# Kernel optimization log

Hardware: AMD Instinct MI355X
Metric: run time of the kernel (lower is better)

Reference implementation:

```python
import jax, jax.numpy as jnp
import numpy as np

MIN_STD = 0.1

def _lin(x, W, b):
    return x @ W.T + b


def setup_inputs() -> dict:
    B, T, H, L, E, A = 256, 128, 2048, 256, 1024, 32
    key = jax.random.key(0)
    ks = jax.random.split(key, 40)
    def w(i, shape, s=0.02):
        return (jax.random.normal(ks[i], shape, jnp.float32) * s)
    z = lambda n: jnp.zeros((n,), jnp.float32)
    return {
        "prev_stochastic_state": w(0, (B, L), 1.0),
        "prev_hidden": w(1, (B, H), 1.0),
        "encoded_obs": w(2, (B, T, E), 1.0),
        "actions": w(3, (B, T, A), 1.0),
        "noise_prior": w(4, (B, T, L), 1.0),
        "noise_post": w(5, (B, T, L), 1.0),
        # fc_embed_state_action
        "W_embed": w(6, (H, L + A)), "b_embed": z(H),
        # GRUCell (torch layout: 3H rows = [r; z; n])
        "W_ih": w(7, (3 * H, H)), "b_ih": z(3 * H),
        "W_hh": w(8, (3 * H, H)), "b_hh": z(3 * H),
        # prior MLP (200-dim) + heads
        "Wp1": w(9, (200, H)), "bp1": z(200),
        "Wp2": w(10, (200, 200)), "bp2": z(200),
        "Wpm": w(11, (L, 200)), "bpm": z(L),
        "Wps": w(12, (L, 200)), "bps": z(L),
        # posterior MLP (200-dim) + heads
        "Wq1": w(13, (200, H + E)), "bq1": z(200),
        "Wq2": w(14, (200, 200)), "bq2": z(200),
        "Wqm": w(15, (L, 200)), "bqm": z(L),
        "Wqs": w(16, (L, 200)), "bqs": z(L),
        # reward head
        "Wr1": w(17, (200, L + H)), "br1": z(200),
        "Wr2": w(18, (200, 200)), "br2": z(200),
        "Wr3": w(19, (1, 200)), "br3": z(1),
    }


def reference(prev_stochastic_state, prev_hidden, encoded_obs, actions,
              noise_prior, noise_post,
              W_embed, b_embed, W_ih, b_ih, W_hh, b_hh,
              Wp1, bp1, Wp2, bp2, Wpm, bpm, Wps, bps,
              Wq1, bq1, Wq2, bq2, Wqm, bqm, Wqs, bqs,
              Wr1, br1, Wr2, br2, Wr3, br3):
    def gru(x, h):
        gi = x @ W_ih.T + b_ih          # [B, 3H]
        gh = h @ W_hh.T + b_hh
        i_r, i_z, i_n = jnp.split(gi, 3, axis=-1)
        h_r, h_z, h_n = jnp.split(gh, 3, axis=-1)
        r = jax.nn.sigmoid(i_r + h_r)
        z = jax.nn.sigmoid(i_z + h_z)
        n = jnp.tanh(i_n + r * h_n)
        return (1.0 - z) * n + z * h

    def step(carry, xs):
        post, h = carry
        enc_t, act_t, np_t, nq_t = xs
        emb = jax.nn.relu(_lin(jnp.concatenate([post, act_t], -1), W_embed, b_embed))
        h = gru(emb, h)
        pf = jax.nn.relu(_lin(jax.nn.relu(_lin(h, Wp1, bp1)), Wp2, bp2))
        pmu = _lin(pf, Wpm, bpm)
        pstd = jax.nn.softplus(_lin(pf, Wps, bps)) + MIN_STD
        prior_s = pmu + pstd * np_t
        qf = jax.nn.relu(_lin(jax.nn.relu(_lin(jnp.concatenate([h, enc_t], -1), Wq1, bq1)), Wq2, bq2))
        qmu = _lin(qf, Wqm, bqm)
        qstd = jax.nn.softplus(_lin(qf, Wqs, bqs)) + MIN_STD
        post = qmu + qstd * nq_t
        rew = _lin(jax.nn.relu(_lin(jax.nn.relu(_lin(jnp.concatenate([post, h], -1), Wr1, br1)), Wr2, br2)), Wr3, br3)
        return (post, h), (prior_s, post, h, pmu, pstd, qmu, qstd, rew)

    xs = (encoded_obs.transpose(1, 0, 2), actions.transpose(1, 0, 2),
          noise_prior.transpose(1, 0, 2), noise_post.transpose(1, 0, 2))
    _, ys = jax.lax.scan(step, (prev_stochastic_state, prev_hidden), xs)
    # scan stacks on axis 0 (time); torch stacks on dim 1 -> swap to [B, T, ...]
    return tuple(jnp.swapaxes(y, 0, 1) for y in ys)
```

## Files before the change

kernel.cpp:

```cpp
#include <hip/hip_runtime.h>
#include <hip/hip_bf16.h>

#define TS 128
#define NB 256
#define HD 2048
#define H3 6144
#define LD 256
#define ED 1024
#define AD 32
#define FD 200
#define KE 288
#define KQ 3072
#define KR 2304
#define MT 32768

typedef __attribute__((ext_vector_type(8))) short short8;
typedef __attribute__((ext_vector_type(4))) float f32x4;

constexpr size_t alup(size_t x) { return (x + 255) & ~size_t(255); }
constexpr size_t O_WE   = 0;
constexpr size_t O_WIH  = alup(O_WE   + 2ull*2048*288);
constexpr size_t O_WHH  = alup(O_WIH  + 2ull*6144*2048);
constexpr size_t O_WQ1  = alup(O_WHH  + 2ull*6144*2048);
constexpr size_t O_WQ2  = alup(O_WQ1  + 2ull*200*3072);
constexpr size_t O_WQMS = alup(O_WQ2  + 2ull*200*200);
constexpr size_t O_WP1  = alup(O_WQMS + 2ull*512*200);
constexpr size_t O_WP2  = alup(O_WP1  + 2ull*200*2048);
constexpr size_t O_WPMS = alup(O_WP2  + 2ull*200*200);
constexpr size_t O_WR1  = alup(O_WPMS + 2ull*512*200);
constexpr size_t O_WR2  = alup(O_WR1  + 2ull*200*2304);
constexpr size_t O_WR3  = alup(O_WR2  + 2ull*200*200);
constexpr size_t O_BQMS = alup(O_WR3  + 2ull*200);
constexpr size_t O_BPMS = alup(O_BQMS + 4ull*512);
constexpr size_t O_POSTB= alup(O_BPMS + 4ull*512);
constexpr size_t O_HBF  = alup(O_POSTB+ 2ull*NB*LD);
constexpr size_t O_HF   = alup(O_HBF  + 2ull*NB*HD);
constexpr size_t O_EMB  = alup(O_HF   + 4ull*NB*HD);
constexpr size_t O_GH   = alup(O_EMB  + 2ull*NB*HD);
constexpr size_t O_Q1P  = alup(O_GH   + 4ull*NB*H3);
constexpr size_t O_Q2   = alup(O_Q1P  + 4ull*16*NB*256);
constexpr size_t O_BARF = alup(O_Q2   + 2ull*NB*FD);
constexpr size_t O_BARC = alup(O_BARF + 4ull*(64*32+64));
constexpr size_t O_P1B  = alup(O_BARC + 4ull*(16*32+64));
constexpr size_t O_P2B  = alup(O_P1B  + 2ull*(size_t)MT*FD);
constexpr size_t O_END  = alup(O_P2B  + 2ull*(size_t)MT*FD);

#define Y0 0ull
#define Y1 8388608ull
#define Y2 16777216ull
#define Y3 83886080ull
#define Y4 92274688ull
#define Y5 100663296ull
#define Y6 109051904ull
#define Y7 117440512ull

__device__ __forceinline__ unsigned short f2bf(float f) {
  union { float f; unsigned u; } v; v.f = f;
  unsigned r = v.u + 0x7fffu + ((v.u >> 16) & 1u);
  return (unsigned short)(r >> 16);
}
__device__ __forceinline__ float bf2f(unsigned short u) {
  union { unsigned u; float f; } v; v.u = ((unsigned)u) << 16;
  return v.f;
}
__device__ __forceinline__ float sigm(float x) { return 1.f / (1.f + __expf(-x)); }
__device__ __forceinline__ float tanh_f(float x) {
  float e = __expf(-2.f * fabsf(x));
  float t = (1.f - e) / (1.f + e);
  return x >= 0.f ? t : -t;
}
__device__ __forceinline__ float softp(float x) { return x > 15.f ? x : log1pf(__expf(x)); }
__device__ __forceinline__ f32x4 z4() { f32x4 z; z[0]=0.f; z[1]=0.f; z[2]=0.f; z[3]=0.f; return z; }

struct SMem {
  alignas(16) short As[64*72];
  alignas(16) short Ws[128*72];
};
struct SMemP {
  alignas(16) short A[2][64*64];
  alignas(16) short W[2][64*64];
};
union SMemU { SMemP p; SMem legacy; };
struct SMemQH {
  alignas(16) short As[64*72];
  alignas(16) short Ws[128*72];
  alignas(16) short q2l[64*264];
};

struct Aseg {
  const char* p0; int lda0; int K0; int f0;
  const char* p1; int lda1; int f1;
  int K;
};

__device__ __forceinline__ void stageA(short* As, const Aseg& a, int m0, int k0) {
  const int t = threadIdx.x;
  const int row = t >> 2;
  const int cb = (t & 3) << 4;
  #pragma unroll
  for (int i = 0; i < 2; ++i) {
    const int c = cb + i * 8;
    const int gk = k0 + c;
    short8 v = {};
    if (gk < a.K) {
      const char* p; long idx; int isf;
      if (gk < a.K0) { p = a.p0; idx = (long)(m0 + row) * a.lda0 + gk; isf = a.f0; }
      else           { p = a.p1; idx = (long)(m0 + row) * a.lda1 + (gk - a.K0); isf = a.f1; }
      if (isf) {
        const float* pf = (const float*)p + idx;
        #pragma unroll
        for (int j = 0; j < 8; ++j) v[j] = (short)f2bf(pf[j]);
      } else {
        v = *(const short8*)((const short*)p + idx);
      }
    }
    *(short8*)&As[row*72 + c] = v;
  }
}

__device__ __forceinline__ void stageW(short* Ws, const short* W, int ldw, int n0, int BN,
                                       int Nmax, int k0, int K) {
  const int nch = BN << 3;
  for (int id = threadIdx.x; id < nch; id += 256) {
    const int row = id >> 3;
    const int c = (id & 7) << 3;
    const int gk = k0 + c;
    int gr = n0 + row; gr = gr < Nmax ? gr : Nmax - 1;
    short8 v = {};
    if (gk < K) v = *(const short8*)(W + (long)gr * ldw + gk);
    *(short8*)&Ws[row*72 + c] = v;
  }
}

__device__ __forceinline__ void stageA_red(short* As, const float* q1p, const float* bq1,
                                           int m0, int k0) {
  const int t = threadIdx.x;
  const int row = t >> 2;
  const int cb = (t & 3) << 4;
  #pragma unroll
  for (int i = 0; i < 2; ++i) {
    const int c = cb + i * 8;
    const int gk = k0 + c;
    short8 v = {};
    if (gk < FD) {
      float s[8];
      #pragma unroll
      for (int j = 0; j < 8; ++j) s[j] = bq1[gk + j];
      for (int ss = 0; ss < 16; ++ss) {
        const float* p = q1p + (size_t)ss * NB * 256 + (size_t)(m0 + row) * 256 + gk;
        #pragma unroll
        for (int j = 0; j < 8; ++j) s[j] += p[j];
      }
      #pragma unroll
      for (int j = 0; j < 8; ++j) v[j] = (short)f2bf(fmaxf(s[j], 0.f));
    }
    *(short8*)&As[row*72 + c] = v;
  }
}

template<int NF>
__device__ __forceinline__ void mma_tile(const short* As, const short* Ws, f32x4 acc[2][NF]) {
  const int lane = threadIdx.x & 63;
  const int w = threadIdx.x >> 6;
  const int wm = (w >> 1) << 5;
  const int wn = (w & 1) * (NF << 4);
  const int lr = lane & 15, lk = (lane >> 4) << 3;
  #pragma unroll
  for (int ks = 0; ks < 2; ++ks) {
    const int ko = ks * 32 + lk;
    short8 a0 = *(const short8*)&As[(wm + lr)*72 + ko];
    short8 a1 = *(const short8*)&As[(wm + 16 + lr)*72 + ko];
    #pragma unroll
    for (int f = 0; f < NF; ++f) {
      short8 b = *(const short8*)&Ws[(wn + f*16 + lr)*72 + ko];
      acc[0][f] = __builtin_amdgcn_mfma_f32_16x16x32_bf16(a0, b, acc[0][f], 0, 0, 0);
      acc[1][f] = __builtin_amdgcn_mfma_f32_16x16x32_bf16(a1, b, acc[1][f], 0, 0, 0);
    }
  }
}

template<int NF>
__device__ __forceinline__ void mma_q2l(const short* q2l, const short* Ws, int k0,
                                        f32x4 acc[2][NF]) {
  const int lane = threadIdx.x & 63;
  const int w = threadIdx.x >> 6;
  const int wm = (w >> 1) << 5;
  const int wn = (w & 1) * (NF << 4);
  const int lr = lane & 15, lk = (lane >> 4) << 3;
  #pragma unroll
  for (int ks = 0; ks < 2; ++ks) {
    const int kl = ks * 32 + lk;
    short8 a0 = *(const short8*)&q2l[(wm + lr)*264 + k0 + kl];
    short8 a1 = *(const short8*)&q2l[(wm + 16 + lr)*264 + k0 + kl];
    #pragma unroll
    for (int f = 0; f < NF; ++f) {
      short8 b = *(const short8*)&Ws[(wn + f*16 + lr)*72 + kl];
      acc[0][f] = __builtin_amdgcn_mfma_f32_16x16x32_bf16(a0, b, acc[0][f], 0, 0, 0);
      acc[1][f] = __builtin_amdgcn_mfma_f32_16x16x32_bf16(a1, b, acc[1][f], 0, 0, 0);
    }
  }
}

template<int NF>
__device__ void run_gemm(SMem& sm, const Aseg& a, const short* W, int ldw, int m0, int n0,
                         int Nmax, f32x4 acc[2][NF], int kb, int ke) {
  for (int k0 = kb; k0 < ke; k0 += 64) {
    __syncthreads();
    stageA(sm.As, a, m0, k0);
    stageW(sm.Ws, W, ldw, n0, NF*32, Nmax, k0, a.K);
    __syncthreads();
    mma_tile<NF>(sm.As, sm.Ws, acc);
  }
}

template<int NF>
__device__ void epi_generic(f32x4 acc[2][NF], int m0, int n0, int Nmax, const float* bias,
                            int relu, float* outF, long rsF, unsigned short* outB, int rsB) {
  const int lane = threadIdx.x & 63;
  const int w = threadIdx.x >> 6;
  const int wm = (w >> 1) << 5, wn = (w & 1) * (NF << 4);
  #pragma unroll
  for (int mt = 0; mt < 2; ++mt)
  #pragma unroll
  for (int f = 0; f < NF; ++f)
  #pragma unroll
  for (int r = 0; r < 4; ++r) {
    const int m = m0 + wm + mt*16 + ((lane >> 4) << 2) + r;
    const int n = n0 + wn + f*16 + (lane & 15);
    if (n < Nmax) {
      float v = acc[mt][f][r];
      if (bias) v += bias[n];
      if (relu) v = fmaxf(v, 0.f);
      if (outF) outF[(long)m * rsF + n] = v;
      if (outB) outB[(long)m * rsB + n] = f2bf(v);
    }
  }
}

template<int NF>
__device__ void epi_q2l(f32x4 acc[2][NF], int n0, const float* bias, short* q2l) {
  const int lane = threadIdx.x & 63;
  const int w = threadIdx.x >> 6;
  const int wm = (w >> 1) << 5, wn = (w & 1) * (NF << 4);
  #pragma unroll
  for (int mt = 0; mt < 2; ++mt)
  #pragma unroll
  for (int f = 0; f < NF; ++f)
  #pragma unroll
  for (int r = 0; r < 4; ++r) {
    const int ml = wm + mt*16 + ((lane >> 4) << 2) + r;
    const int n = n0 + wn + f*16 + (lane & 15);
    if (n < FD) {
      float v = fmaxf(acc[mt][f][r] + bias[n], 0.f);
      q2l[ml*264 + n] = (short)f2bf(v);
    }
  }
}

template<int NF>
__device__ void epi_heads(f32x4 acc[2][NF], int m0, int n0, const float* biasI,
                          const float* noise, long rs, float* outMu, float* outStd,
                          float* outComb, unsigned short* postbf) {
  const int lane = threadIdx.x & 63;
  const int w = threadIdx.x >> 6;
  const int wm = (w >> 1) << 5, wn = (w & 1) * (NF << 4);
  #pragma unroll
  for (int mt = 0; mt < 2; ++mt)
  #pragma unroll
  for (int f = 0; f < NF; ++f)
  #pragma unroll
  for (int r = 0; r < 4; ++r) {
    const int m = m0 + wm + mt*16 + ((lane >> 4) << 2) + r;
    const int n = n0 + wn + f*16 + (lane & 15);
    float v = acc[mt][f][r] + biasI[n];
    if (n & 1) v = softp(v) + 0.1f;
    float partner = __shfl_xor(v, 1);
    const int l = n >> 1;
    if (n & 1) {
      outStd[(long)m * rs + l] = v;
    } else {
      outMu[(long)m * rs + l] = v;
      float comb = v + partner * noise[(long)m * rs + l];
      outComb[(long)m * rs + l] = comb;
      if (postbf) postbf[m * LD + l] = f2bf(comb);
    }
  }
}

__device__ __forceinline__ void gl_lds16(const void* g, void* l) {
  __builtin_amdgcn_global_load_lds(
      (const __attribute__((address_space(1))) unsigned int*)g,
      (__attribute__((address_space(3))) unsigned int*)l, 16, 0, 0);
}

#define PIPE_BAR() do { \
    asm volatile("s_waitcnt vmcnt(0)" ::: "memory"); \
    __builtin_amdgcn_s_barrier(); \
    __builtin_amdgcn_sched_barrier(0); \
  } while (0)

__device__ __forceinline__ void stage_pipe_rows(short* dst, const short* g, long ldw,
                                                int rbase, int k0) {
  const int w = threadIdx.x >> 6, l = threadIdx.x & 63;
  #pragma unroll
  for (int i = 0; i < 2; ++i) {
    const int inst = w*2 + i;
    const int row = inst*8 + (l >> 3);
    const int sc = (l & 7) ^ (row & 7);
    gl_lds16(g + (long)(rbase + row) * ldw + k0 + sc*8, dst + inst*512);
  }
}
__device__ __forceinline__ void stage_pipe_gi(short* dst, const short* W, int j0, int k0) {
  const int w = threadIdx.x >> 6, l = threadIdx.x & 63;
  #pragma unroll
  for (int i = 0; i < 2; ++i) {
    const int inst = w*2 + i;
    const int row = inst*8 + (l >> 3);
    const int g = (row >> 4) % 3;
    const int sc = (l & 7) ^ (row & 7);
    gl_lds16(W + (long)(g*2048 + j0 + (row & 15)) * 2048 + k0 + sc*8, dst + inst*512);
  }
}

template<int NF>
__device__ __forceinline__ void mma_swz(const short* As, const short* Ws, f32x4 acc[2][NF]) {
  const int lane = threadIdx.x & 63, w = threadIdx.x >> 6;
  const int wm = (w >> 1) << 5, wn = (w & 1) * (NF << 4);
  const int lr = lane & 15, lk = (lane >> 4) << 3;
  #pragma unroll
  for (int ks = 0; ks < 2; ++ks) {
    const int ko = ks*32 + lk; const int ca = ko >> 3;
    const int ra0 = wm + lr, ra1 = wm + 16 + lr;
    short8 a0 = *(const short8*)&As[ra0*64 + ((ca ^ (ra0 & 7)) << 3)];
    short8 a1 = *(const short8*)&As[ra1*64 + ((ca ^ (ra1 & 7)) << 3)];
    #pragma unroll
    for (int f = 0; f < NF; ++f) {
      const int rb = wn + f*16 + lr;
      short8 b = *(const short8*)&Ws[rb*64 + ((ca ^ (rb & 7)) << 3)];
      acc[0][f] = __builtin_amdgcn_mfma_f32_16x16x32_bf16(a0, b, acc[0][f], 0, 0, 0);
      acc[1][f] = __builtin_amdgcn_mfma_f32_16x16x32_bf16(a1, b, acc[1][f], 0, 0, 0);
    }
  }
}

__device__ __forceinline__ void mma_gi(const short* As, const short* Ws, f32x4 acc[3]) {
  const int lane = threadIdx.x & 63, w = threadIdx.x >> 6;
  const int lr = lane & 15, lk = (lane >> 4) << 3;
  #pragma unroll
  for (int ks = 0; ks < 2; ++ks) {
    const int ko = ks*32 + lk; const int ca = ko >> 3;
    const int ra = w*16 + lr;
    short8 av = *(const short8*)&As[ra*64 + ((ca ^ (ra & 7)) << 3)];
    #pragma unroll
    for (int f = 0; f < 3; ++f) {
      const int rb = f*16 + lr;
      short8 bv = *(const short8*)&Ws[rb*64 + ((ca ^ (rb & 7)) << 3)];
      acc[f] = __builtin_amdgcn_mfma_f32_16x16x32_bf16(av, bv, acc[f], 0, 0, 0);
    }
  }
}

struct CArgs {
  char* ws;
  const float* enc; const float* act; const float* nq;
  const float* b_e; const float* b_ih; const float* b_hh;
  const float* b_q1; const float* b_q2;
  float* y1; float* y2; float* y5; float* y6;
};

__device__ void emb_tile(SMem& sm, const CArgs& A, int id, int t) {
  const int mi = id & 3, ni = id >> 2;
  const int m0 = mi << 6, n0 = ni << 7;
  Aseg a{A.ws + O_POSTB, LD, LD, 0, (const char*)(A.act + (size_t)t*AD), TS*AD, 1, KE};
  f32x4 acc[2][4];
  for (int i=0;i<2;++i) for (int j=0;j<4;++j) acc[i][j] = z4();
  run_gemm<4>(sm, a, (const short*)(A.ws + O_WE), KE, m0, n0, HD, acc, 0, 320);
  epi_generic<4>(acc, m0, n0, HD, A.b_e, 1, nullptr, 0, (unsigned short*)(A.ws + O_EMB), HD);
}

__device__ void gh_tile_pipe(SMemP& sm, const CArgs& A, int id) {
  const int xcd = id & 7, local = id >> 3;
  const int mi = local & 3, nio = local >> 2;
  const int m0 = mi << 6, n0 = xcd*768 + nio*64;
  const short* hB  = (const short*)(A.ws + O_HBF);
  const short* Whh = (const short*)(A.ws + O_WHH);
  f32x4 acc[2][2];
  for (int i=0;i<2;++i) for (int j=0;j<2;++j) acc[i][j] = z4();
  int cur = 0;
  stage_pipe_rows(sm.A[0], hB, HD, m0, 0);
  stage_pipe_rows(sm.W[0], Whh, HD, n0, 0);
  PIPE_BAR();
  for (int k0 = 0; k0 < HD; k0 += 64) {
    if (k0 + 64 < HD) {
      stage_pipe_rows(sm.A[cur^1], hB, HD, m0, k0 + 64);
      stage_pipe_rows(sm.W[cur^1], Whh, HD, n0, k0 + 64);
    }
    mma_swz<2>(sm.A[cur], sm.W[cur], acc);
    PIPE_BAR();
    cur ^= 1;
  }
  epi_generic<2>(acc, m0, n0, H3, A.b_hh, 0, (float*)(A.ws + O_GH), H3, nullptr, 0);
}

__device__ void gi_tile_pipe(SMemP& sm, const CArgs& A, int id, int t) {
  const int xcd = id & 7, local = id >> 3;
  const int mi = local & 3, jl = local >> 2;
  const int m0 = mi << 6, j0 = xcd*256 + jl*16;
  const short* eB  = (const short*)(A.ws + O_EMB);
  const short* Wih = (const short*)(A.ws + O_WIH);
  f32x4 acc[3]; acc[0] = z4(); acc[1] = z4(); acc[2] = z4();
  int cur = 0;
  stage_pipe_rows(sm.A[0], eB, HD, m0, 0);
  stage_pipe_gi(sm.W[0], Wih, j0, 0);
  PIPE_BAR();
  for (int k0 = 0; k0 < HD; k0 += 64) {
    if (k0 + 64 < HD) {
      stage_pipe_rows(sm.A[cur^1], eB, HD, m0, k0 + 64);
      stage_pipe_gi(sm.W[cur^1], Wih, j0, k0 + 64);
    }
    mma_gi(sm.A[cur], sm.W[cur], acc);
    PIPE_BAR();
    cur ^= 1;
  }
  const int lane = threadIdx.x & 63, w = threadIdx.x >> 6;
  const int lr = lane & 15;
  const int j = j0 + lr;
  float* hF = (float*)(A.ws + O_HF);
  unsigned short* hB = (unsigned short*)(A.ws + O_HBF);
  const float* gh = (const float*)(A.ws + O_GH);
  #pragma unroll
  for (int r = 0; r < 4; ++r) {
    const int m = m0 + w*16 + ((lane >> 4) << 2) + r;
    const float* g = gh + (size_t)m * H3;
    const float ir = acc[0][r] + A.b_ih[j]        + g[j];
    const float iz = acc[1][r] + A.b_ih[HD + j]   + g[HD + j];
    const float in_ = acc[2][r] + A.b_ih[2*HD + j];
    const float rr = sigm(ir), zz = sigm(iz);
    const float nn = tanh_f(in_ + rr * g[2*HD + j]);
    const float hv = (1.f - zz) * nn + zz * hF[(size_t)m*HD + j];
    hF[(size_t)m*HD + j] = hv;
    hB[(size_t)m*HD + j] = f2bf(hv);
    A.y2[(size_t)m * (TS*HD) + (size_t)t*HD + j] = hv;
  }
}

__device__ void q1_tile(SMem& sm, const CArgs& A, int id, int t) {
  const int s = id >> 3, rest = id & 7;
  const int mi = rest & 3, ni = rest >> 2;
  const int m0 = mi << 6, n0 = ni << 7;
  Aseg a{A.ws + O_HBF, HD, HD, 0, (const char*)(A.enc + (size_t)t*ED), TS*ED, 1, KQ};
  f32x4 acc[2][4];
  for (int i=0;i<2;++i) for (int j=0;j<4;++j) acc[i][j] = z4();
  run_gemm<4>(sm, a, (const short*)(A.ws + O_WQ1), KQ, m0, n0, FD, acc, s*192, s*192+192);
  epi_generic<4>(acc, m0, n0, FD, nullptr, 0,
                 (float*)(A.ws + O_Q1P) + (size_t)s*NB*256, 256, nullptr, 0);
}

__global__ __launch_bounds__(256, 2) void k_step1(CArgs A, int t) {
  __shared__ SMemU sm;
  if (blockIdx.x < 384) gh_tile_pipe(sm.p, A, blockIdx.x);
  else                  emb_tile(sm.legacy, A, blockIdx.x - 384, t);
}
__global__ __launch_bounds__(256, 2) void k_gi(CArgs A, int t) {
  __shared__ SMemP sm;
  gi_tile_pipe(sm, A, blockIdx.x, t);
}
__global__ __launch_bounds__(256, 2) void k_q1(CArgs A, int t) {
  __shared__ SMem sm;
  q1_tile(sm, A, blockIdx.x, t);
}

__global__ __launch_bounds__(256, 2) void k_q2h(CArgs A, int t) {
  __shared__ SMemQH sm;
  const int id = blockIdx.x;
  const int mi = id & 3, qi = id >> 2;
  const int m0 = mi << 6;

  const short* Wq2 = (const short*)(A.ws + O_WQ2);
  #pragma unroll 1
  for (int np = 0; np < 2; ++np) {
    f32x4 acc[2][4];
    for (int i=0;i<2;++i) for (int j=0;j<4;++j) acc[i][j] = z4();
    for (int k0 = 0; k0 < 256; k0 += 64) {
      __syncthreads();
      stageA_red(sm.As, (const float*)(A.ws + O_Q1P), A.b_q1, m0, k0);
      stageW(sm.Ws, Wq2, FD, np*128, 128, FD, k0, FD);
      __syncthreads();
      mma_tile<4>(sm.As, sm.Ws, acc);
    }
    epi_q2l<4>(acc, np*128, A.b_q2, sm.q2l);
  }
  for (int i = threadIdx.x; i < 64*64; i += 256)
    sm.q2l[(i >> 6)*264 + 200 + (i & 63)] = 0;
  __syncthreads();

  const short* Wqms = (const short*)(A.ws + O_WQMS);
  f32x4 acc[2][4];
  for (int i=0;i<2;++i) for (int j=0;j<4;++j) acc[i][j] = z4();
  for (int k0 = 0; k0 < 256; k0 += 64) {
    __syncthreads();
    stageW(sm.Ws, Wqms, FD, qi*128, 128, 512, k0, FD);
    __syncthreads();
    mma_q2l<4>(sm.q2l, sm.Ws, k0, acc);
  }
  epi_heads<4>(acc, m0, qi*128, (const float*)(A.ws + O_BQMS),
               A.nq + (size_t)t*LD, (long)TS*LD,
               A.y5 + (size_t)t*LD, A.y6 + (size_t)t*LD, A.y1 + (size_t)t*LD,
               (unsigned short*)(A.ws + O_POSTB));
}

__global__ void k_init(char* ws, const float* prevs, const float* prevh,
  const float* We, const float* Wih, const float* Whh,
  const float* Wp1, const float* Wp2, const float* Wpm, const float* Wps,
  const float* Wq1, const float* Wq2, const float* Wqm, const float* Wqs,
  const float* Wr1, const float* Wr2, const float* Wr3,
  const float* bpm, const float* bps, const float* bqm, const float* bqs) {
  const size_t stride = (size_t)gridDim.x * blockDim.x;
  for (size_t i = (size_t)blockIdx.x*blockDim.x + threadIdx.x; i < 12582912ull; i += stride) {
    ((unsigned short*)(ws + O_WIH))[i] = f2bf(Wih[i]);
    ((unsigned short*)(ws + O_WHH))[i] = f2bf(Whh[i]);
    if (i < 589824)  ((unsigned short*)(ws + O_WE))[i]  = f2bf(We[i]);
    if (i < 614400)  ((unsigned short*)(ws + O_WQ1))[i] = f2bf(Wq1[i]);
    if (i < 409600)  ((unsigned short*)(ws + O_WP1))[i] = f2bf(Wp1[i]);
    if (i < 460800)  ((unsigned short*)(ws + O_WR1))[i] = f2bf(Wr1[i]);
    if (i < 40000) {
      ((unsigned short*)(ws + O_WQ2))[i] = f2bf(Wq2[i]);
      ((unsigned short*)(ws + O_WP2))[i] = f2bf(Wp2[i]);
      ((unsigned short*)(ws + O_WR2))[i] = f2bf(Wr2[i]);
    }
    if (i < 200) ((unsigned short*)(ws + O_WR3))[i] = f2bf(Wr3[i]);
    if (i < 102400) {
      const int r = (int)(i / 200), c = (int)(i % 200);
      ((unsigned short*)(ws + O_WQMS))[i] = f2bf(((r & 1) ? Wqs : Wqm)[(r >> 1)*200 + c]);
      ((unsigned short*)(ws + O_WPMS))[i] = f2bf(((r & 1) ? Wps : Wpm)[(r >> 1)*200 + c]);
    }
    if (i < 512) {
      ((float*)(ws + O_BQMS))[i] = ((i & 1) ? bqs : bqm)[i >> 1];
      ((float*)(ws + O_BPMS))[i] = ((i & 1) ? bps : bpm)[i >> 1];
    }
    if (i < 65536) ((unsigned short*)(ws + O_POSTB))[i] = f2bf(prevs[i]);
    if (i < 524288) {
      ((unsigned short*)(ws + O_HBF))[i] = f2bf(prevh[i]);
      ((float*)(ws + O_HF))[i] = prevh[i];
    }
  }
}

__global__ __launch_bounds__(256, 2) void k_big(int mode, char* ws,
  const float* y1, const float* y2, float* y0, float* y3, float* y4,
  const float* npn, const float* bp1, const float* bp2, const float* br1, const float* br2) {
  __shared__ SMem sm;
  if (mode == 2) {
    for (int tile = blockIdx.x; tile < 2048; tile += gridDim.x) {
      const int mi = tile >> 2, ni = tile & 3;
      const int m0 = mi << 6, n0 = ni << 7;
      Aseg a{ws + O_P2B, FD, FD, 0, nullptr, 0, 0, FD};
      f32x4 acc[2][4];
      for (int i=0;i<2;++i) for (int j=0;j<4;++j) acc[i][j] = z4();
      run_gemm<4>(sm, a, (const short*)(ws + O_WPMS), FD, m0, n0, 512, acc, 0, 256);
      epi_heads<4>(acc, m0, n0, (const float*)(ws + O_BPMS), npn, 256, y3, y4, y0, nullptr);
    }
    return;
  }
  for (int tile = blockIdx.x; tile < 1024; tile += gridDim.x) {
    const int mi = tile >> 1, ni = tile & 1;
    const int m0 = mi << 6, n0 = ni << 7;
    Aseg a; const short* W; const float* bias;
    if (mode == 0)      { a = {(const char*)y2, HD, HD, 1, nullptr, 0, 0, HD}; W = (const short*)(ws + O_WP1); bias = bp1; }
    else if (mode == 1) { a = {ws + O_P1B, FD, FD, 0, nullptr, 0, 0, FD};      W = (const short*)(ws + O_WP2); bias = bp2; }
    else if (mode == 3) { a = {(const char*)y1, LD, LD, 1, (const char*)y2, HD, 1, KR}; W = (const short*)(ws + O_WR1); bias = br1; }
    else                { a = {ws + O_P1B, FD, FD, 0, nullptr, 0, 0, FD};      W = (const short*)(ws + O_WR2); bias = br2; }
    f32x4 acc[2][4];
    for (int i=0;i<2;++i) for (int j=0;j<4;++j) acc[i][j] = z4();
    const int ke = (a.K + 63) & ~63;
    run_gemm<4>(sm, a, W, a.K, m0, n0, FD, acc, 0, ke);
    unsigned short* outp = (unsigned short*)(ws + ((mode == 0 || mode == 3) ? O_P1B : O_P2B));
    epi_generic<4>(acc, m0, n0, FD, bias, 1, nullptr, 0, outp, FD);
  }
}

__global__ void k_r3(char* ws, const float* br3, float* y7) {
  __shared__ float w3[200];
  for (int i = threadIdx.x; i < 200; i += 256) w3[i] = bf2f(((unsigned short*)(ws + O_WR3))[i]);
  __syncthreads();
  const int m = blockIdx.x * 256 + threadIdx.x;
  const unsigned short* r2 = (const unsigned short*)(ws + O_P2B) + (size_t)m * FD;
  float s = br3[0];
  for (int k = 0; k < FD; k += 8) {
    short8 v = *(const short8*)(r2 + k);
    #pragma unroll
    for (int j = 0; j < 8; ++j) s += bf2f((unsigned short)v[j]) * w3[k + j];
  }
  y7[m] = s;
}

extern "C" void kernel_launch(void* const* d_in, const int* in_sizes, int n_in,
                              void* d_out, int out_size, void* d_ws, size_t ws_size,
                              hipStream_t stream) {
  (void)in_sizes; (void)n_in; (void)out_size; (void)ws_size;
  char* ws = (char*)d_ws;
  #define FIN(i) ((const float*)d_in[i])
  float* out = (float*)d_out;
  float* y0 = out + Y0; float* y1 = out + Y1; float* y2 = out + Y2; float* y3 = out + Y3;
  float* y4 = out + Y4; float* y5 = out + Y5; float* y6 = out + Y6; float* y7 = out + Y7;

  k_init<<<2048, 256, 0, stream>>>(ws, FIN(0), FIN(1), FIN(6), FIN(8), FIN(10),
    FIN(12), FIN(14), FIN(16), FIN(18), FIN(20), FIN(22), FIN(24), FIN(26),
    FIN(28), FIN(30), FIN(32), FIN(17), FIN(19), FIN(25), FIN(27));

  CArgs ca;
  ca.ws = ws; ca.enc = FIN(2); ca.act = FIN(3); ca.nq = FIN(5);
  ca.b_e = FIN(7); ca.b_ih = FIN(9); ca.b_hh = FIN(11); ca.b_q1 = FIN(21); ca.b_q2 = FIN(23);
  ca.y1 = y1; ca.y2 = y2; ca.y5 = y5; ca.y6 = y6;

  for (int t = 0; t < TS; ++t) {
    k_step1<<<448, 256, 0, stream>>>(ca, t);
    k_gi   <<<512, 256, 0, stream>>>(ca, t);
    k_q1   <<<128, 256, 0, stream>>>(ca, t);
    k_q2h  <<<16,  256, 0, stream>>>(ca, t);
  }

  k_big<<<2048, 256, 0, stream>>>(0, ws, y1, y2, y0, y3, y4, FIN(4), FIN(13), FIN(15), FIN(29), FIN(31));
  k_big<<<2048, 256, 0, stream>>>(1, ws, y1, y2, y0, y3, y4, FIN(4), FIN(13), FIN(15), FIN(29), FIN(31));
  k_big<<<2048, 256, 0, stream>>>(2, ws, y1, y2, y0, y3, y4, FIN(4), FIN(13), FIN(15), FIN(29), FIN(31));
  k_big<<<2048, 256, 0, stream>>>(3, ws, y1, y2, y0, y3, y4, FIN(4), FIN(13), FIN(15), FIN(29), FIN(31));
  k_big<<<2048, 256, 0, stream>>>(4, ws, y1, y2, y0, y3, y4, FIN(4), FIN(13), FIN(15), FIN(29), FIN(31));
  k_r3<<<128, 256, 0, stream>>>(ws, FIN(33), y7);
}
```

Baseline: 18.01 ms.

## Restructure per-step kernels to overlap next-step gh and embedding with posterior tail

Reorganizes the per-timestep launch sequence from four kernels into three. The q1 split-K drops from 16 to 4 partial slices, and the q1 tiles share a launch with the next step's W_hh·h GEMM tiles. The posterior head kernel now computes q2 once per block and then all four head chunks, writing outputs from one block column only. It then computes the next step's embedding GEMM, removing the separate step1 launch inside the loop. The aim is fewer launches and better use of the GPU during the serial recurrence. The cost is redundant q2/head compute across the 32 tail blocks, and correctness depends on the new cross-kernel ordering (e.g. gh reading hidden state before it is updated).

New measurement: 25.64 ms. 42.4% more time.

```diff
diff --git a/kernel.cpp b/kernel.cpp
--- a/kernel.cpp
+++ b/kernel.cpp
@@ -132,8 +132,8 @@
   }
 }
 
-__device__ __forceinline__ void stageA_red(short* As, const float* q1p, const float* bq1,
-                                           int m0, int k0) {
+__device__ __forceinline__ void stageA_red4(short* As, const float* q1p, const float* bq1,
+                                            int m0, int k0) {
   const int t = threadIdx.x;
   const int row = t >> 2;
   const int cb = (t & 3) << 4;
@@ -146,7 +146,8 @@
       float s[8];
       #pragma unroll
       for (int j = 0; j < 8; ++j) s[j] = bq1[gk + j];
-      for (int ss = 0; ss < 16; ++ss) {
+      #pragma unroll
+      for (int ss = 0; ss < 4; ++ss) {
         const float* p = q1p + (size_t)ss * NB * 256 + (size_t)(m0 + row) * 256 + gk;
         #pragma unroll
         for (int j = 0; j < 8; ++j) s[j] += p[j];
@@ -202,14 +203,14 @@
 }
 
 template<int NF>
-__device__ void run_gemm(SMem& sm, const Aseg& a, const short* W, int ldw, int m0, int n0,
-                         int Nmax, f32x4 acc[2][NF], int kb, int ke) {
+__device__ void run_gemm(short* As, short* Ws, const Aseg& a, const short* W, int ldw,
+                         int m0, int n0, int Nmax, f32x4 acc[2][NF], int kb, int ke) {
   for (int k0 = kb; k0 < ke; k0 += 64) {
     __syncthreads();
-    stageA(sm.As, a, m0, k0);
-    stageW(sm.Ws, W, ldw, n0, NF*32, Nmax, k0, a.K);
+    stageA(As, a, m0, k0);
+    stageW(Ws, W, ldw, n0, NF*32, Nmax, k0, a.K);
     __syncthreads();
-    mma_tile<NF>(sm.As, sm.Ws, acc);
+    mma_tile<NF>(As, Ws, acc);
   }
 }
 
@@ -260,7 +261,7 @@
 template<int NF>
 __device__ void epi_heads(f32x4 acc[2][NF], int m0, int n0, const float* biasI,
                           const float* noise, long rs, float* outMu, float* outStd,
-                          float* outComb, unsigned short* postbf) {
+                          float* outComb, unsigned short* postbf, int wy) {
   const int lane = threadIdx.x & 63;
   const int w = threadIdx.x >> 6;
   const int wm = (w >> 1) << 5, wn = (w & 1) * (NF << 4);
@@ -277,11 +278,13 @@
     float partner = __shfl_xor(v, 1);
     const int l = n >> 1;
     if (n & 1) {
-      outStd[(long)m * rs + l] = v;
+      if (wy) outStd[(long)m * rs + l] = v;
     } else {
-      outMu[(long)m * rs + l] = v;
       float comb = v + partner * noise[(long)m * rs + l];
-      outComb[(long)m * rs + l] = comb;
+      if (wy) {
+        outMu[(long)m * rs + l] = v;
+        outComb[(long)m * rs + l] = comb;
+      }
       if (postbf) postbf[m * LD + l] = f2bf(comb);
     }
   }
@@ -374,7 +377,7 @@
   Aseg a{A.ws + O_POSTB, LD, LD, 0, (const char*)(A.act + (size_t)t*AD), TS*AD, 1, KE};
   f32x4 acc[2][4];
   for (int i=0;i<2;++i) for (int j=0;j<4;++j) acc[i][j] = z4();
-  run_gemm<4>(sm, a, (const short*)(A.ws + O_WE), KE, m0, n0, HD, acc, 0, 320);
+  run_gemm<4>(sm.As, sm.Ws, a, (const short*)(A.ws + O_WE), KE, m0, n0, HD, acc, 0, 320);
   epi_generic<4>(acc, m0, n0, HD, A.b_e, 1, nullptr, 0, (unsigned short*)(A.ws + O_EMB), HD);
 }
 
@@ -444,14 +447,15 @@
   }
 }
 
-__device__ void q1_tile(SMem& sm, const CArgs& A, int id, int t) {
+__device__ void q1_tile4(SMem& sm, const CArgs& A, int id, int t) {
   const int s = id >> 3, rest = id & 7;
   const int mi = rest & 3, ni = rest >> 2;
   const int m0 = mi << 6, n0 = ni << 7;
   Aseg a{A.ws + O_HBF, HD, HD, 0, (const char*)(A.enc + (size_t)t*ED), TS*ED, 1, KQ};
   f32x4 acc[2][4];
   for (int i=0;i<2;++i) for (int j=0;j<4;++j) acc[i][j] = z4();
-  run_gemm<4>(sm, a, (const short*)(A.ws + O_WQ1), KQ, m0, n0, FD, acc, s*192, s*192+192);
+  run_gemm<4>(sm.As, sm.Ws, a, (const short*)(A.ws + O_WQ1), KQ, m0, n0, FD, acc,
+              s*768, s*768+768);
   epi_generic<4>(acc, m0, n0, FD, nullptr, 0,
                  (float*)(A.ws + O_Q1P) + (size_t)s*NB*256, 256, nullptr, 0);
 }
@@ -465,48 +469,72 @@
   __shared__ SMemP sm;
   gi_tile_pipe(sm, A, blockIdx.x, t);
 }
-__global__ __launch_bounds__(256, 2) void k_q1(CArgs A, int t) {
-  __shared__ SMem sm;
-  q1_tile(sm, A, blockIdx.x, t);
-}
-
-__global__ __launch_bounds__(256, 2) void k_q2h(CArgs A, int t) {
+__global__ __launch_bounds__(256, 2) void k_mid(CArgs A, int t) {
+  __shared__ SMemU sm;
+  if (blockIdx.x < 32) { q1_tile4(sm.legacy, A, blockIdx.x, t); return; }
+  if (t + 1 >= TS) return;
+  gh_tile_pipe(sm.p, A, blockIdx.x - 32);
+}
+
+__global__ __launch_bounds__(256, 2) void k_tail(CArgs A, int t) {
   __shared__ SMemQH sm;
   const int id = blockIdx.x;
-  const int mi = id & 3, qi = id >> 2;
+  const int mi = id & 3, ci = id >> 2;
   const int m0 = mi << 6;
 
   const short* Wq2 = (const short*)(A.ws + O_WQ2);
+  {
+    f32x4 acc0[2][4], acc1[2][4];
+    for (int i=0;i<2;++i) for (int j=0;j<4;++j) { acc0[i][j] = z4(); acc1[i][j] = z4(); }
+    for (int k0 = 0; k0 < 256; k0 += 64) {
+      __syncthreads();
+      stageA_red4(sm.As, (const float*)(A.ws + O_Q1P), A.b_q1, m0, k0);
+      stageW(sm.Ws, Wq2, FD, 0, 128, FD, k0, FD);
+      __syncthreads();
+      mma_tile<4>(sm.As, sm.Ws, acc0);
+      __syncthreads();
+      stageW(sm.Ws, Wq2, FD, 128, 128, FD, k0, FD);
+      __syncthreads();
+      mma_tile<4>(sm.As, sm.Ws, acc1);
+    }
+    epi_q2l<4>(acc0, 0, A.b_q2, sm.q2l);
+    epi_q2l<4>(acc1, 128, A.b_q2, sm.q2l);
+  }
+  for (int i = threadIdx.x; i < 64*64; i += 256)
+    sm.q2l[(i >> 6)*264 + 200 + (i & 63)] = 0;
+  __syncthreads();
+
+  const short* Wqms = (const short*)(A.ws + O_WQMS);
+  unsigned short* postb = (unsigned short*)(A.ws + O_POSTB);
   #pragma unroll 1
-  for (int np = 0; np < 2; ++np) {
+  for (int qn = 0; qn < 4; ++qn) {
     f32x4 acc[2][4];
     for (int i=0;i<2;++i) for (int j=0;j<4;++j) acc[i][j] = z4();
     for (int k0 = 0; k0 < 256; k0 += 64) {
       __syncthreads();
-      stageA_red(sm.As, (const float*)(A.ws + O_Q1P), A.b_q1, m0, k0);
-      stageW(sm.Ws, Wq2, FD, np*128, 128, FD, k0, FD);
+      stageW(sm.Ws, Wqms, FD, qn*128, 128, 512, k0, FD);
       __syncthreads();
-      mma_tile<4>(sm.As, sm.Ws, acc);
-    }
-    epi_q2l<4>(acc, np*128, A.b_q2, sm.q2l);
-  }
-  for (int i = threadIdx.x; i < 64*64; i += 256)
-    sm.q2l[(i >> 6)*264 + 200 + (i & 63)] = 0;
+      mma_q2l<4>(sm.q2l, sm.Ws, k0, acc);
+    }
+    epi_heads<4>(acc, m0, qn*128, (const float*)(A.ws + O_BQMS),
+                 A.nq + (size_t)t*LD, (long)TS*LD,
+                 A.y5 + (size_t)t*LD, A.y6 + (size_t)t*LD, A.y1 + (size_t)t*LD,
+                 postb, ci == 0);
+  }
+
+  if (t + 1 >= TS) return;
+  asm volatile("s_waitcnt vmcnt(0)" ::: "memory");
   __syncthreads();
-
-  const short* Wqms = (const short*)(A.ws + O_WQMS);
-  f32x4 acc[2][4];
-  for (int i=0;i<2;++i) for (int j=0;j<4;++j) acc[i][j] = z4();
-  for (int k0 = 0; k0 < 256; k0 += 64) {
-    __syncthreads();
-    stageW(sm.Ws, Wqms, FD, qi*128, 128, 512, k0, FD);
-    __syncthreads();
-    mma_q2l<4>(sm.q2l, sm.Ws, k0, acc);
-  }
-  epi_heads<4>(acc, m0, qi*128, (const float*)(A.ws + O_BQMS),
-               A.nq + (size_t)t*LD, (long)TS*LD,
-               A.y5 + (size_t)t*LD, A.y6 + (size_t)t*LD, A.y1 + (size_t)t*LD,
-               (unsigned short*)(A.ws + O_POSTB));
+  Aseg a{A.ws + O_POSTB, LD, LD, 0, (const char*)(A.act + (size_t)(t+1)*AD), TS*AD, 1, KE};
+  unsigned short* embB = (unsigned short*)(A.ws + O_EMB);
+  #pragma unroll 1
+  for (int cc = 0; cc < 2; ++cc) {
+    const int n0 = ci*256 + cc*128;
+    f32x4 acc[2][4];
+    for (int i=0;i<2;++i) for (int j=0;j<4;++j) acc[i][j] = z4();
+    run_gemm<4>(sm.As, sm.Ws, a, (const short*)(A.ws + O_WE), KE, m0, n0, HD, acc, 0, 320);
+    epi_generic<4>(acc, m0, n0, HD, A.b_e, 1, nullptr, 0, embB, HD);
+  }
 }
 
 __global__ void k_init(char* ws, const float* prevs, const float* prevh,
@@ -557,8 +585,9 @@
       Aseg a{ws + O_P2B, FD, FD, 0, nullptr, 0, 0, FD};
       f32x4 acc[2][4];
       for (int i=0;i<2;++i) for (int j=0;j<4;++j) acc[i][j] = z4();
-      run_gemm<4>(sm, a, (const short*)(ws + O_WPMS), FD, m0, n0, 512, acc, 0, 256);
-      epi_heads<4>(acc, m0, n0, (const float*)(ws + O_BPMS), npn, 256, y3, y4, y0, nullptr);
+      run_gemm<4>(sm.As, sm.Ws, a, (const short*)(ws + O_WPMS), FD, m0, n0, 512, acc, 0, 256);
+      epi_heads<4>(acc, m0, n0, (const float*)(ws + O_BPMS), npn, 256, y3, y4, y0,
+                   nullptr, 1);
     }
     return;
   }
@@ -573,7 +602,7 @@
     f32x4 acc[2][4];
     for (int i=0;i<2;++i) for (int j=0;j<4;++j) acc[i][j] = z4();
     const int ke = (a.K + 63) & ~63;
-    run_gemm<4>(sm, a, W, a.K, m0, n0, FD, acc, 0, ke);
+    run_gemm<4>(sm.As, sm.Ws, a, W, a.K, m0, n0, FD, acc, 0, ke);
     unsigned short* outp = (unsigned short*)(ws + ((mode == 0 || mode == 3) ? O_P1B : O_P2B));
     epi_generic<4>(acc, m0, n0, FD, bias, 1, nullptr, 0, outp, FD);
   }
@@ -613,11 +642,11 @@
   ca.b_e = FIN(7); ca.b_ih = FIN(9); ca.b_hh = FIN(11); ca.b_q1 = FIN(21); ca.b_q2 = FIN(23);
   ca.y1 = y1; ca.y2 = y2; ca.y5 = y5; ca.y6 = y6;
 
+  k_step1<<<448, 256, 0, stream>>>(ca, 0);
   for (int t = 0; t < TS; ++t) {
-    k_step1<<<448, 256, 0, stream>>>(ca, t);
-    k_gi   <<<512, 256, 0, stream>>>(ca, t);
-    k_q1   <<<128, 256, 0, stream>>>(ca, t);
-    k_q2h  <<<16,  256, 0, stream>>>(ca, t);
+    k_gi  <<<512, 256, 0, stream>>>(ca, t);
+    k_mid <<<416, 256, 0, stream>>>(ca, t);
+    k_tail<<<32,  256, 0, stream>>>(ca, t);
   }
 
   k_big<<<2048, 256, 0, stream>>>(0, ws, y1, y2, y0, y3, y4, FIN(4), FIN(13), FIN(15), FIN(29), FIN(31));
```

## Triple-buffer GRU GEMMs and overlap next-step gh with q1 in fused launch

Applied to the files above, without the earlier changes.

Switches the gh and gi pipelined GEMMs from double to triple buffering, with vmcnt-based partial waits so two stages of loads stay in flight. Moves the next step's W_hh·h GEMM into a new k_mid kernel that runs alongside the q1 GEMM, and splits embedding into its own k_emb launch. The q1 K-split is cut from 16 to 4 slices, which shrinks the partial-sum reduction, and k_q2h now computes both N halves in one pass over the reduced A tile. The cost is more LDS per block, a restructured per-step launch schedule with cross-step dependencies, and fewer q1 blocks, so less parallelism on that GEMM.

Measured after the change: 15.07 ms. 16.3% less time.

```diff
diff --git a/kernel.cpp b/kernel.cpp
--- a/kernel.cpp
+++ b/kernel.cpp
@@ -77,8 +77,8 @@
   alignas(16) short Ws[128*72];
 };
 struct SMemP {
-  alignas(16) short A[2][64*64];
-  alignas(16) short W[2][64*64];
+  alignas(16) short A[3][64*64];
+  alignas(16) short W[3][64*64];
 };
 union SMemU { SMemP p; SMem legacy; };
 struct SMemQH {
@@ -132,8 +132,8 @@
   }
 }
 
-__device__ __forceinline__ void stageA_red(short* As, const float* q1p, const float* bq1,
-                                           int m0, int k0) {
+__device__ __forceinline__ void stageA_red4(short* As, const float* q1p, const float* bq1,
+                                            int m0, int k0) {
   const int t = threadIdx.x;
   const int row = t >> 2;
   const int cb = (t & 3) << 4;
@@ -146,7 +146,8 @@
       float s[8];
       #pragma unroll
       for (int j = 0; j < 8; ++j) s[j] = bq1[gk + j];
-      for (int ss = 0; ss < 16; ++ss) {
+      #pragma unroll
+      for (int ss = 0; ss < 4; ++ss) {
         const float* p = q1p + (size_t)ss * NB * 256 + (size_t)(m0 + row) * 256 + gk;
         #pragma unroll
         for (int j = 0; j < 8; ++j) s[j] += p[j];
@@ -293,12 +294,6 @@
       (__attribute__((address_space(3))) unsigned int*)l, 16, 0, 0);
 }
 
-#define PIPE_BAR() do { \
-    asm volatile("s_waitcnt vmcnt(0)" ::: "memory"); \
-    __builtin_amdgcn_s_barrier(); \
-    __builtin_amdgcn_sched_barrier(0); \
-  } while (0)
-
 __device__ __forceinline__ void stage_pipe_rows(short* dst, const short* g, long ldw,
                                                 int rbase, int k0) {
   const int w = threadIdx.x >> 6, l = threadIdx.x & 63;
@@ -386,18 +381,27 @@
   const short* Whh = (const short*)(A.ws + O_WHH);
   f32x4 acc[2][2];
   for (int i=0;i<2;++i) for (int j=0;j<2;++j) acc[i][j] = z4();
-  int cur = 0;
-  stage_pipe_rows(sm.A[0], hB, HD, m0, 0);
-  stage_pipe_rows(sm.W[0], Whh, HD, n0, 0);
-  PIPE_BAR();
-  for (int k0 = 0; k0 < HD; k0 += 64) {
-    if (k0 + 64 < HD) {
-      stage_pipe_rows(sm.A[cur^1], hB, HD, m0, k0 + 64);
-      stage_pipe_rows(sm.W[cur^1], Whh, HD, n0, k0 + 64);
-    }
-    mma_swz<2>(sm.A[cur], sm.W[cur], acc);
-    PIPE_BAR();
-    cur ^= 1;
+  stage_pipe_rows(sm.A[0], hB, HD, m0, 0);   stage_pipe_rows(sm.W[0], Whh, HD, n0, 0);
+  stage_pipe_rows(sm.A[1], hB, HD, m0, 64);  stage_pipe_rows(sm.W[1], Whh, HD, n0, 64);
+  #pragma unroll 1
+  for (int idx = 0; idx < 32; ++idx) {
+    const int buf = idx % 3;
+    if (idx + 2 < 32) {
+      const int nb = (idx + 2) % 3;
+      stage_pipe_rows(sm.A[nb], hB, HD, m0, (idx+2)*64);
+      stage_pipe_rows(sm.W[nb], Whh, HD, n0, (idx+2)*64);
+      asm volatile("s_waitcnt vmcnt(8)" ::: "memory");
+    } else if (idx + 1 < 32) {
+      asm volatile("s_waitcnt vmcnt(4)" ::: "memory");
+    } else {
+      asm volatile("s_waitcnt vmcnt(0)" ::: "memory");
+    }
+    __builtin_amdgcn_s_barrier();
+    __builtin_amdgcn_sched_barrier(0);
+    mma_swz<2>(sm.A[buf], sm.W[buf], acc);
+    asm volatile("s_waitcnt lgkmcnt(0)" ::: "memory");
+    __builtin_amdgcn_sched_barrier(0);
+    __builtin_amdgcn_s_barrier();
   }
   epi_generic<2>(acc, m0, n0, H3, A.b_hh, 0, (float*)(A.ws + O_GH), H3, nullptr, 0);
 }
@@ -409,18 +413,27 @@
   const short* eB  = (const short*)(A.ws + O_EMB);
   const short* Wih = (const short*)(A.ws + O_WIH);
   f32x4 acc[3]; acc[0] = z4(); acc[1] = z4(); acc[2] = z4();
-  int cur = 0;
-  stage_pipe_rows(sm.A[0], eB, HD, m0, 0);
-  stage_pipe_gi(sm.W[0], Wih, j0, 0);
-  PIPE_BAR();
-  for (int k0 = 0; k0 < HD; k0 += 64) {
-    if (k0 + 64 < HD) {
-      stage_pipe_rows(sm.A[cur^1], eB, HD, m0, k0 + 64);
-      stage_pipe_gi(sm.W[cur^1], Wih, j0, k0 + 64);
-    }
-    mma_gi(sm.A[cur], sm.W[cur], acc);
-    PIPE_BAR();
-    cur ^= 1;
+  stage_pipe_rows(sm.A[0], eB, HD, m0, 0);   stage_pipe_gi(sm.W[0], Wih, j0, 0);
+  stage_pipe_rows(sm.A[1], eB, HD, m0, 64);  stage_pipe_gi(sm.W[1], Wih, j0, 64);
+  #pragma unroll 1
+  for (int idx = 0; idx < 32; ++idx) {
+    const int buf = idx % 3;
+    if (idx + 2 < 32) {
+      const int nb = (idx + 2) % 3;
+      stage_pipe_rows(sm.A[nb], eB, HD, m0, (idx+2)*64);
+      stage_pipe_gi(sm.W[nb], Wih, j0, (idx+2)*64);
+      asm volatile("s_waitcnt vmcnt(8)" ::: "memory");
+    } else if (idx + 1 < 32) {
+      asm volatile("s_waitcnt vmcnt(4)" ::: "memory");
+    } else {
+      asm volatile("s_waitcnt vmcnt(0)" ::: "memory");
+    }
+    __builtin_amdgcn_s_barrier();
+    __builtin_amdgcn_sched_barrier(0);
+    mma_gi(sm.A[buf], sm.W[buf], acc);
+    asm volatile("s_waitcnt lgkmcnt(0)" ::: "memory");
+    __builtin_amdgcn_sched_barrier(0);
+    __builtin_amdgcn_s_barrier();
   }
   const int lane = threadIdx.x & 63, w = threadIdx.x >> 6;
   const int lr = lane & 15;
@@ -444,14 +457,14 @@
   }
 }
 
-__device__ void q1_tile(SMem& sm, const CArgs& A, int id, int t) {
+__device__ void q1_tile4(SMem& sm, const CArgs& A, int id, int t) {
   const int s = id >> 3, rest = id & 7;
   const int mi = rest & 3, ni = rest >> 2;
   const int m0 = mi << 6, n0 = ni << 7;
   Aseg a{A.ws + O_HBF, HD, HD, 0, (const char*)(A.enc + (size_t)t*ED), TS*ED, 1, KQ};
   f32x4 acc[2][4];
   for (int i=0;i<2;++i) for (int j=0;j<4;++j) acc[i][j] = z4();
-  run_gemm<4>(sm, a, (const short*)(A.ws + O_WQ1), KQ, m0, n0, FD, acc, s*192, s*192+192);
+  run_gemm<4>(sm, a, (const short*)(A.ws + O_WQ1), KQ, m0, n0, FD, acc, s*768, s*768+768);
   epi_generic<4>(acc, m0, n0, FD, nullptr, 0,
                  (float*)(A.ws + O_Q1P) + (size_t)s*NB*256, 256, nullptr, 0);
 }
@@ -465,11 +478,12 @@
   __shared__ SMemP sm;
   gi_tile_pipe(sm, A, blockIdx.x, t);
 }
-__global__ __launch_bounds__(256, 2) void k_q1(CArgs A, int t) {
-  __shared__ SMem sm;
-  q1_tile(sm, A, blockIdx.x, t);
-}
-
+__global__ __launch_bounds__(256, 2) void k_mid(CArgs A, int t) {
+  __shared__ SMemU sm;
+  if (blockIdx.x < 32) { q1_tile4(sm.legacy, A, blockIdx.x, t); return; }
+  if (t + 1 >= TS) return;
+  gh_tile_pipe(sm.p, A, blockIdx.x - 32);
+}
 __global__ __launch_bounds__(256, 2) void k_q2h(CArgs A, int t) {
   __shared__ SMemQH sm;
   const int id = blockIdx.x;
@@ -477,18 +491,22 @@
   const int m0 = mi << 6;
 
   const short* Wq2 = (const short*)(A.ws + O_WQ2);
-  #pragma unroll 1
-  for (int np = 0; np < 2; ++np) {
-    f32x4 acc[2][4];
-    for (int i=0;i<2;++i) for (int j=0;j<4;++j) acc[i][j] = z4();
+  {
+    f32x4 acc0[2][4], acc1[2][4];
+    for (int i=0;i<2;++i) for (int j=0;j<4;++j) { acc0[i][j] = z4(); acc1[i][j] = z4(); }
     for (int k0 = 0; k0 < 256; k0 += 64) {
       __syncthreads();
-      stageA_red(sm.As, (const float*)(A.ws + O_Q1P), A.b_q1, m0, k0);
-      stageW(sm.Ws, Wq2, FD, np*128, 128, FD, k0, FD);
+      stageA_red4(sm.As, (const float*)(A.ws + O_Q1P), A.b_q1, m0, k0);
+      stageW(sm.Ws, Wq2, FD, 0, 128, FD, k0, FD);
       __syncthreads();
-      mma_tile<4>(sm.As, sm.Ws, acc);
-    }
-    epi_q2l<4>(acc, np*128, A.b_q2, sm.q2l);
+      mma_tile<4>(sm.As, sm.Ws, acc0);
+      __syncthreads();
+      stageW(sm.Ws, Wq2, FD, 128, 128, FD, k0, FD);
+      __syncthreads();
+      mma_tile<4>(sm.As, sm.Ws, acc1);
+    }
+    epi_q2l<4>(acc0, 0, A.b_q2, sm.q2l);
+    epi_q2l<4>(acc1, 128, A.b_q2, sm.q2l);
   }
   for (int i = threadIdx.x; i < 64*64; i += 256)
     sm.q2l[(i >> 6)*264 + 200 + (i & 63)] = 0;
@@ -507,6 +525,10 @@
                A.nq + (size_t)t*LD, (long)TS*LD,
                A.y5 + (size_t)t*LD, A.y6 + (size_t)t*LD, A.y1 + (size_t)t*LD,
                (unsigned short*)(A.ws + O_POSTB));
+}
+__global__ __launch_bounds__(256, 2) void k_emb(CArgs A, int t) {
+  __shared__ SMem sm;
+  emb_tile(sm, A, blockIdx.x, t);
 }
 
 __global__ void k_init(char* ws, const float* prevs, const float* prevh,
@@ -613,11 +635,12 @@
   ca.b_e = FIN(7); ca.b_ih = FIN(9); ca.b_hh = FIN(11); ca.b_q1 = FIN(21); ca.b_q2 = FIN(23);
   ca.y1 = y1; ca.y2 = y2; ca.y5 = y5; ca.y6 = y6;
 
+  k_step1<<<448, 256, 0, stream>>>(ca, 0);
   for (int t = 0; t < TS; ++t) {
-    k_step1<<<448, 256, 0, stream>>>(ca, t);
-    k_gi   <<<512, 256, 0, stream>>>(ca, t);
-    k_q1   <<<128, 256, 0, stream>>>(ca, t);
-    k_q2h  <<<16,  256, 0, stream>>>(ca, t);
+    k_gi  <<<512, 256, 0, stream>>>(ca, t);
+    k_mid <<<416, 256, 0, stream>>>(ca, t);
+    k_q2h <<<16,  256, 0, stream>>>(ca, t);
+    if (t + 1 < TS) k_emb<<<64, 256, 0, stream>>>(ca, t + 1);
   }
 
   k_big<<<2048, 256, 0, stream>>>(0, ws, y1, y2, y0, y3, y4, FIN(4), FIN(13), FIN(15), FIN(29), FIN(31));
```
